# Optimization experiments

Hardware: AMD Instinct MI355X
Metric: run time of the kernel (lower is better)

## Reference

```python
import jax, jax.numpy as jnp
import numpy as np

N_HEAD = 16
N_EMBD = 1024
SPARSE_BLOCK = 64  # band width: keys j with i-64 <= j <= i are visible
B, T = 2, 2048


def setup_inputs() -> dict:
    key = jax.random.key(0)
    ks = jax.random.split(key, 5)
    C = N_EMBD
    scale = 0.02
    return {
        "x": jax.random.normal(ks[0], (B, T, C), dtype=jnp.float32),
        "Wqkv": jax.random.normal(ks[1], (C, 3 * C), dtype=jnp.float32) * scale,
        "bqkv": jnp.zeros((3 * C,), dtype=jnp.float32),
        "Wproj": jax.random.normal(ks[2], (C, C), dtype=jnp.float32) * scale,
        "bproj": jnp.zeros((C,), dtype=jnp.float32),
    }


def reference(x, Wqkv, bqkv, Wproj, bproj):
    Bz, Tz, C = x.shape
    H, D = N_HEAD, C // N_HEAD
    qkv = x @ Wqkv + bqkv                       # [B,T,3C]
    q, k, v = jnp.split(qkv, 3, axis=-1)

    def heads(t):  # [B,T,C] -> [B,H,T,D]
        return t.reshape(Bz, Tz, H, D).transpose(0, 2, 1, 3)
    q, k, v = heads(q), heads(k), heads(v)

    scale = 1.0 / jnp.sqrt(jnp.float32(D))
    att = jnp.einsum("bhtd,bhsd->bhts", q, k) * scale  # [B,H,T,T]

    # causal + local band mask: key j visible to query i iff i-64 <= j <= i
    i = jnp.arange(Tz)[:, None]
    j = jnp.arange(Tz)[None, :]
    mask = (j <= i) & (j >= i - SPARSE_BLOCK)           # [T,T] bool
    att = jnp.where(mask[None, None], att, -jnp.inf)
    att = jax.nn.softmax(att, axis=-1)

    y = jnp.einsum("bhts,bhsd->bhtd", att, v)           # [B,H,T,D]
    y = y.transpose(0, 2, 1, 3).reshape(Bz, Tz, C)
    return y @ Wproj + bproj
```

## Files before the change

kernel.cpp:

```cpp
#include <hip/hip_runtime.h>
#include <hip/hip_bf16.h>
#include <math.h>

#define N_HEAD 16
#define N_EMBD 1024
#define HEADD  64
#define BANDW  64
#define BB     2
#define TT     2048

typedef __attribute__((ext_vector_type(8))) short bf16x8;
typedef __attribute__((ext_vector_type(4))) float f32x4;

__device__ __forceinline__ ushort f2b(float f) {
    __hip_bfloat16 h = __float2bfloat16(f);
    union { __hip_bfloat16 h; ushort u; } cv; cv.h = h; return cv.u;
}
__device__ __forceinline__ float b2f(ushort u) { return __uint_as_float(((unsigned)u) << 16); }

#define GLOAD16(gp, lp) \
    __builtin_amdgcn_global_load_lds((const __attribute__((address_space(1))) void*)(gp), \
                                     (__attribute__((address_space(3))) void*)(lp), 16, 0, 0)

__global__ __launch_bounds__(256) void k_prep(
    const float* __restrict__ x, ushort* __restrict__ xb,
    const float* __restrict__ Wqkv, ushort* __restrict__ wqkvT,
    const float* __restrict__ Wproj, ushort* __restrict__ wprojT)
{
    __shared__ float tile[32][33];
    int bid = blockIdx.x;
    int t = threadIdx.x;
    if (bid < 4096) {
        int i = bid * 256 + t;
        float4 v = reinterpret_cast<const float4*>(x)[i];
        ushort4 o;
        o.x = f2b(v.x); o.y = f2b(v.y); o.z = f2b(v.z); o.w = f2b(v.w);
        reinterpret_cast<ushort4*>(xb)[i] = o;
        return;
    }
    const float* in; ushort* out; int R, C, bx, by;
    if (bid < 4096 + 3072) {
        int b2 = bid - 4096;
        in = Wqkv; out = wqkvT; R = 1024; C = 3072;
        bx = b2 % 96; by = b2 / 96;
    } else {
        int b3 = bid - 7168;
        in = Wproj; out = wprojT; R = 1024; C = 1024;
        bx = b3 & 31; by = b3 >> 5;
    }
    int tx = t & 31, ty = t >> 5;
    int c0 = bx * 32, r0 = by * 32;
    for (int rr = ty; rr < 32; rr += 8)
        tile[rr][tx] = in[(size_t)(r0 + rr) * C + (c0 + tx)];
    __syncthreads();
    for (int cc = ty; cc < 32; cc += 8)
        out[(size_t)(c0 + cc) * R + (r0 + tx)] = f2b(tile[tx][cc]);
}

template <bool OUT_BF16>
__global__ __launch_bounds__(512, 4) void k_gemm1(
    const ushort* __restrict__ A, const ushort* __restrict__ BT,
    const float* __restrict__ bias, void* __restrict__ Cout,
    int M, int N, int K)
{
    __shared__ __align__(16) char lds[81920];
    const int K2 = K * 2;
    int t = threadIdx.x, lane = t & 63, w = t >> 6;
    int wm = w >> 2, wn = w & 3;
    int lr = lane & 15, kg = lane >> 4;

    int nbx = N / 192;
    int cpx = gridDim.x >> 3;
    int wg = blockIdx.x;
    int wgid = (wg & 7) * cpx + (wg >> 3);
    int bx = wgid % nbx, by = wgid / nbx;
    int row0 = by * 128, col0 = bx * 192;

    size_t sA0, sA1, sB0, sB1, sB2;
    {
        int o = w * 2048 + lane * 16;
        int r = o >> 7, c = ((o >> 4) - r) & 7;
        sA0 = (size_t)r * K2 + c * 16;
        o += 1024; r = o >> 7; c = ((o >> 4) - r) & 7;
        sA1 = (size_t)r * K2 + c * 16;
        int ob = w * 3072 + lane * 16;
        int rb = ob >> 7, cb = ((ob >> 4) - rb) & 7;
        sB0 = (size_t)rb * K2 + cb * 16;
        ob += 1024; rb = ob >> 7; cb = ((ob >> 4) - rb) & 7;
        sB1 = (size_t)rb * K2 + cb * 16;
        ob += 1024; rb = ob >> 7; cb = ((ob >> 4) - rb) & 7;
        sB2 = (size_t)rb * K2 + cb * 16;
    }
    const char* gA = (const char*)A  + (size_t)row0 * K2;
    const char* gB = (const char*)BT + (size_t)col0 * K2;

    int offA[4][2], offB[3][2];
#pragma unroll
    for (int m = 0; m < 4; ++m) {
        int rr = wm * 64 + m * 16 + lr;
#pragma unroll
        for (int ks = 0; ks < 2; ++ks)
            offA[m][ks] = rr * 128 + (((ks * 4 + kg) + rr) & 7) * 16;
    }
#pragma unroll
    for (int n = 0; n < 3; ++n) {
        int rr = wn * 48 + n * 16 + lr;
#pragma unroll
        for (int ks = 0; ks < 2; ++ks)
            offB[n][ks] = rr * 128 + (((ks * 4 + kg) + rr) & 7) * 16;
    }

    f32x4 acc[4][3];
#pragma unroll
    for (int i = 0; i < 4; ++i)
#pragma unroll
        for (int j = 0; j < 3; ++j) { f32x4 z = {0.f, 0.f, 0.f, 0.f}; acc[i][j] = z; }

#define STAGE1(BUF, TI) do { \
        char* _db = lds + (BUF) * 40960; \
        const char* _ga = gA + (size_t)(TI) * 128; \
        const char* _gb = gB + (size_t)(TI) * 128; \
        GLOAD16(_ga + sA0, _db + w * 2048); \
        GLOAD16(_ga + sA1, _db + w * 2048 + 1024); \
        GLOAD16(_gb + sB0, _db + 16384 + w * 3072); \
        GLOAD16(_gb + sB1, _db + 16384 + w * 3072 + 1024); \
        GLOAD16(_gb + sB2, _db + 16384 + w * 3072 + 2048); \
    } while (0)

    int nt = K >> 6;
    STAGE1(0, 0);
    STAGE1(1, 1);
    asm volatile("s_waitcnt vmcnt(5)" ::: "memory");
    __builtin_amdgcn_s_barrier();

#pragma unroll 2
    for (int tt = 0; tt < nt; ++tt) {
        int cur = tt & 1;
        const char* bufb = lds + cur * 40960;
        bf16x8 af[4][2], bfr[3][2];
#pragma unroll
        for (int ks = 0; ks < 2; ++ks) {
#pragma unroll
            for (int m = 0; m < 4; ++m)
                af[m][ks] = *(const bf16x8*)(bufb + offA[m][ks]);
#pragma unroll
            for (int n = 0; n < 3; ++n)
                bfr[n][ks] = *(const bf16x8*)(bufb + 16384 + offB[n][ks]);
        }
        asm volatile("s_waitcnt lgkmcnt(0)" ::: "memory");
        __builtin_amdgcn_sched_barrier(0);
        __builtin_amdgcn_s_barrier();
        if (tt + 2 < nt) STAGE1(cur, tt + 2);
#pragma unroll
        for (int ks = 0; ks < 2; ++ks)
#pragma unroll
            for (int m = 0; m < 4; ++m)
#pragma unroll
                for (int n = 0; n < 3; ++n)
                    acc[m][n] = __builtin_amdgcn_mfma_f32_16x16x32_bf16(
                        af[m][ks], bfr[n][ks], acc[m][n], 0, 0, 0);
        if (tt + 2 < nt)
            asm volatile("s_waitcnt vmcnt(5)" ::: "memory");
        else
            asm volatile("s_waitcnt vmcnt(0)" ::: "memory");
        __builtin_amdgcn_s_barrier();
    }
#undef STAGE1

#pragma unroll
    for (int m = 0; m < 4; ++m) {
        int growb = row0 + wm * 64 + m * 16 + kg * 4;
#pragma unroll
        for (int n = 0; n < 3; ++n) {
            int gcol = col0 + wn * 48 + n * 16 + lr;
            float bv = bias ? bias[gcol] : 0.f;
#pragma unroll
            for (int e = 0; e < 4; ++e) {
                float val = acc[m][n][e] + bv;
                if (OUT_BF16)
                    ((ushort*)Cout)[(size_t)(growb + e) * N + gcol] = f2b(val);
                else
                    ((float*)Cout)[(size_t)(growb + e) * N + gcol] = val;
            }
        }
    }
}

template <bool OUT_BF16>
__global__ __launch_bounds__(256, 3) void k_gemm2(
    const ushort* __restrict__ A, const ushort* __restrict__ BT,
    const float* __restrict__ bias, void* __restrict__ Cout,
    int M, int N, int K)
{
    __shared__ __align__(16) char lds[2 * 24576];
    const int K2 = K * 2;
    int t = threadIdx.x, lane = t & 63, w = t >> 6;
    int wm = w >> 1, wn = w & 1;
    int lr = lane & 15, kg = lane >> 4;

    int nbx = N >> 6;
    int cpx = gridDim.x >> 3;
    int wg = blockIdx.x;
    int wgid = (wg & 7) * cpx + (wg >> 3);
    int bx = wgid % nbx, by = wgid / nbx;
    int row0 = by * 128, col0 = bx * 64;

    size_t sA[4], sB[2];
#pragma unroll
    for (int u = 0; u < 4; ++u) {
        int o = w * 4096 + u * 1024 + lane * 16;
        int r = o >> 7, c = ((o >> 4) - r) & 7;
        sA[u] = (size_t)r * K2 + c * 16;
    }
#pragma unroll
    for (int u = 0; u < 2; ++u) {
        int o = w * 2048 + u * 1024 + lane * 16;
        int r = o >> 7, c = ((o >> 4) - r) & 7;
        sB[u] = (size_t)r * K2 + c * 16;
    }
    const char* gA = (const char*)A  + (size_t)row0 * K2;
    const char* gB = (const char*)BT + (size_t)col0 * K2;

    int offA[4][2], offB[2][2];
#pragma unroll
    for (int m = 0; m < 4; ++m) {
        int rr = wm * 64 + m * 16 + lr;
#pragma unroll
        for (int ks = 0; ks < 2; ++ks)
            offA[m][ks] = rr * 128 + (((ks * 4 + kg) + rr) & 7) * 16;
    }
#pragma unroll
    for (int n = 0; n < 2; ++n) {
        int rr = wn * 32 + n * 16 + lr;
#pragma unroll
        for (int ks = 0; ks < 2; ++ks)
            offB[n][ks] = rr * 128 + (((ks * 4 + kg) + rr) & 7) * 16;
    }

    f32x4 acc[4][2];
#pragma unroll
    for (int i = 0; i < 4; ++i)
#pragma unroll
        for (int j = 0; j < 2; ++j) { f32x4 z = {0.f, 0.f, 0.f, 0.f}; acc[i][j] = z; }

#define STAGE2(BUF, TI) do { \
        char* _db = lds + (BUF) * 24576; \
        const char* _ga = gA + (size_t)(TI) * 128; \
        const char* _gb = gB + (size_t)(TI) * 128; \
        GLOAD16(_ga + sA[0], _db + w * 4096); \
        GLOAD16(_ga + sA[1], _db + w * 4096 + 1024); \
        GLOAD16(_ga + sA[2], _db + w * 4096 + 2048); \
        GLOAD16(_ga + sA[3], _db + w * 4096 + 3072); \
        GLOAD16(_gb + sB[0], _db + 16384 + w * 2048); \
        GLOAD16(_gb + sB[1], _db + 16384 + w * 2048 + 1024); \
    } while (0)

    int nt = K >> 6;
    STAGE2(0, 0);
    STAGE2(1, 1);
    asm volatile("s_waitcnt vmcnt(6)" ::: "memory");
    __builtin_amdgcn_s_barrier();

#pragma unroll 2
    for (int tt = 0; tt < nt; ++tt) {
        int cur = tt & 1;
        const char* bufb = lds + cur * 24576;
        bf16x8 af[4][2], bfr[2][2];
#pragma unroll
        for (int ks = 0; ks < 2; ++ks) {
#pragma unroll
            for (int m = 0; m < 4; ++m)
                af[m][ks] = *(const bf16x8*)(bufb + offA[m][ks]);
#pragma unroll
            for (int n = 0; n < 2; ++n)
                bfr[n][ks] = *(const bf16x8*)(bufb + 16384 + offB[n][ks]);
        }
        asm volatile("s_waitcnt lgkmcnt(0)" ::: "memory");
        __builtin_amdgcn_sched_barrier(0);
        __builtin_amdgcn_s_barrier();
        if (tt + 2 < nt) STAGE2(cur, tt + 2);
#pragma unroll
        for (int ks = 0; ks < 2; ++ks)
#pragma unroll
            for (int m = 0; m < 4; ++m)
#pragma unroll
                for (int n = 0; n < 2; ++n)
                    acc[m][n] = __builtin_amdgcn_mfma_f32_16x16x32_bf16(
                        af[m][ks], bfr[n][ks], acc[m][n], 0, 0, 0);
        if (tt + 2 < nt)
            asm volatile("s_waitcnt vmcnt(6)" ::: "memory");
        else
            asm volatile("s_waitcnt vmcnt(0)" ::: "memory");
        __builtin_amdgcn_s_barrier();
    }
#undef STAGE2

#pragma unroll
    for (int m = 0; m < 4; ++m) {
        int growb = row0 + wm * 64 + m * 16 + kg * 4;
#pragma unroll
        for (int n = 0; n < 2; ++n) {
            int gcol = col0 + wn * 32 + n * 16 + lr;
            float bv = bias ? bias[gcol] : 0.f;
#pragma unroll
            for (int e = 0; e < 4; ++e) {
                float val = acc[m][n][e] + bv;
                if (OUT_BF16)
                    ((ushort*)Cout)[(size_t)(growb + e) * N + gcol] = f2b(val);
                else
                    ((float*)Cout)[(size_t)(growb + e) * N + gcol] = val;
            }
        }
    }
}

__global__ __launch_bounds__(256) void k_attn(const ushort* __restrict__ qkv,
                                              ushort* __restrict__ y) {
    __shared__ __align__(16) ushort Ks[128 * 64];
    __shared__ ushort Vt[64][136];
    __shared__ ushort Ps[64][136];

    const int R3 = 3 * N_EMBD;
    int bid = blockIdx.x;
    int l  = (bid & 7) * 128 + (bid >> 3);
    int qt = l & 31;
    int h  = (l >> 5) & (N_HEAD - 1);
    int b  = l >> 9;
    int i0 = qt * 64;
    int j0 = i0 - BANDW;
    int hc = h * HEADD;

    int t    = threadIdx.x;
    int lane = t & 63;
    int wq   = t >> 6;
    int lr   = lane & 15;
    int kg   = lane >> 4;

    const ushort* kbase_g = qkv + (size_t)b * TT * R3 + N_EMBD + hc;
#pragma unroll
    for (int rnd = 0; rnd < 4; ++rnd) {
        int o = wq * 4096 + rnd * 1024 + lane * 16;
        int row  = o >> 7;
        int cblk = (((o >> 4) & 7) - row) & 7;
        int j = j0 + row; if (j < 0) j = 0;
        GLOAD16((const char*)(kbase_g + (size_t)j * R3) + cblk * 16,
                (char*)Ks + wq * 4096 + rnd * 1024);
    }

    {
        int row  = t >> 1;
        int part = t & 1;
        int j = j0 + row;
        if (j >= 0) {
            const ushort* vrow = qkv + (size_t)(b * TT + j) * R3 + 2 * N_EMBD + hc + part * 32;
#pragma unroll
            for (int c = 0; c < 4; ++c) {
                uint4 vv = reinterpret_cast<const uint4*>(vrow)[c];
                const ushort* pv = (const ushort*)&vv;
                int dbase = part * 32 + c * 8;
#pragma unroll
                for (int e = 0; e < 8; ++e)
                    Vt[dbase + e][row] = pv[e];
            }
        } else {
#pragma unroll
            for (int c = 0; c < 4; ++c) {
                int dbase = part * 32 + c * 8;
#pragma unroll
                for (int e = 0; e < 8; ++e)
                    Vt[dbase + e][row] = 0;
            }
        }
    }

    const ushort* qbase = qkv + (size_t)(b * TT + i0 + wq * 16 + lr) * R3 + hc;
    bf16x8 aq0 = *reinterpret_cast<const bf16x8*>(qbase + kg * 8);
    bf16x8 aq1 = *reinterpret_cast<const bf16x8*>(qbase + 32 + kg * 8);

    __syncthreads();

    f32x4 s[8];
#pragma unroll
    for (int nt = 0; nt < 8; ++nt) { f32x4 z = {0.f, 0.f, 0.f, 0.f}; s[nt] = z; }
#pragma unroll
    for (int nt = 0; nt < 8; ++nt) {
        int row = nt * 16 + lr;
        const char* kr = (const char*)Ks + row * 128;
        bf16x8 kb0 = *(const bf16x8*)(kr + (((kg)     + row) & 7) * 16);
        bf16x8 kb1 = *(const bf16x8*)(kr + (((4 + kg) + row) & 7) * 16);
        s[nt] = __builtin_amdgcn_mfma_f32_16x16x32_bf16(aq0, kb0, s[nt], 0, 0, 0);
        s[nt] = __builtin_amdgcn_mfma_f32_16x16x32_bf16(aq1, kb1, s[nt], 0, 0, 0);
    }

    float mx[4] = {-INFINITY, -INFINITY, -INFINITY, -INFINITY};
#pragma unroll
    for (int nt = 0; nt < 8; ++nt) {
        int kc = nt * 16 + lr;
#pragma unroll
        for (int e = 0; e < 4; ++e) {
            int qr = wq * 16 + kg * 4 + e;
            bool valid = (kc >= qr) && (kc <= qr + BANDW) && (j0 + kc >= 0);
            float v = s[nt][e] * 0.125f;
            s[nt][e] = valid ? v : -INFINITY;
            mx[e] = fmaxf(mx[e], s[nt][e]);
        }
    }
#pragma unroll
    for (int e = 0; e < 4; ++e) {
#pragma unroll
        for (int m = 1; m <= 8; m <<= 1)
            mx[e] = fmaxf(mx[e], __shfl_xor(mx[e], m, 64));
    }
    float sm[4] = {0.f, 0.f, 0.f, 0.f};
#pragma unroll
    for (int nt = 0; nt < 8; ++nt) {
        int kc = nt * 16 + lr;
#pragma unroll
        for (int e = 0; e < 4; ++e) {
            float p = __expf(s[nt][e] - mx[e]);
            sm[e] += p;
            Ps[wq * 16 + kg * 4 + e][kc] = f2b(p);
        }
    }
#pragma unroll
    for (int e = 0; e < 4; ++e) {
#pragma unroll
        for (int m = 1; m <= 8; m <<= 1)
            sm[e] += __shfl_xor(sm[e], m, 64);
    }

    f32x4 o[4];
#pragma unroll
    for (int vt = 0; vt < 4; ++vt) { f32x4 z = {0.f, 0.f, 0.f, 0.f}; o[vt] = z; }
#pragma unroll
    for (int ks = 0; ks < 4; ++ks) {
        bf16x8 pa = *reinterpret_cast<const bf16x8*>(&Ps[wq * 16 + lr][ks * 32 + kg * 8]);
#pragma unroll
        for (int vt = 0; vt < 4; ++vt) {
            bf16x8 vb = *reinterpret_cast<const bf16x8*>(&Vt[vt * 16 + lr][ks * 32 + kg * 8]);
            o[vt] = __builtin_amdgcn_mfma_f32_16x16x32_bf16(pa, vb, o[vt], 0, 0, 0);
        }
    }

    float inv[4];
#pragma unroll
    for (int e = 0; e < 4; ++e) inv[e] = 1.f / sm[e];

#pragma unroll
    for (int vt = 0; vt < 4; ++vt) {
#pragma unroll
        for (int e = 0; e < 4; ++e) {
            int qr = wq * 16 + kg * 4 + e;
            y[(size_t)(b * TT + i0 + qr) * N_EMBD + hc + vt * 16 + lr] =
                f2b(o[vt][e] * inv[e]);
        }
    }
}

extern "C" void kernel_launch(void* const* d_in, const int* in_sizes, int n_in,
                              void* d_out, int out_size, void* d_ws, size_t ws_size,
                              hipStream_t stream) {
    const float* x     = (const float*)d_in[0];
    const float* Wqkv  = (const float*)d_in[1];
    const float* bqkv  = (const float*)d_in[2];
    const float* Wproj = (const float*)d_in[3];
    const float* bproj = (const float*)d_in[4];
    float* out = (float*)d_out;

    const int M  = BB * TT;
    const int C  = N_EMBD;
    const int N1 = 3 * C;

    char* ws = (char*)d_ws;
    ushort* xb     = (ushort*)ws; ws += (size_t)M  * C * 2;
    ushort* wqkvT  = (ushort*)ws; ws += (size_t)N1 * C * 2;
    ushort* wprojT = (ushort*)ws; ws += (size_t)C  * C * 2;
    ushort* qkvb   = (ushort*)ws; ws += (size_t)M  * N1 * 2;
    ushort* yb     = (ushort*)ws; ws += (size_t)M  * C * 2;

    k_prep<<<8192, 256, 0, stream>>>(x, xb, Wqkv, wqkvT, Wproj, wprojT);
    {
        int nwg = (M / 128) * (N1 / 192);
        k_gemm1<true><<<nwg, 512, 0, stream>>>(xb, wqkvT, bqkv, (void*)qkvb, M, N1, C);
    }
    k_attn<<<BB * N_HEAD * (TT / 64), 256, 0, stream>>>(qkvb, yb);
    {
        int nwg = (M / 128) * (C / 64);
        k_gemm2<false><<<nwg, 256, 0, stream>>>(yb, wprojT, bproj, (void*)out, M, C, C);
    }
}
```

Before: 68.58 us.

## Fuse fp32-to-bf16 conversion of x into QKV GEMM A-tile loading

The separate pass that converts x to bf16 in k_prep is removed. The QKV GEMM now loads fp32 x directly into registers, converts it to bf16, and writes it to LDS while B still streams through global_load_lds. The output tile shrinks from 128x192 to 128x128 to make room in LDS and registers, which increases the workgroup count. This saves a full read and write of the bf16 copy of x, at the cost of reading twice as many bytes for A in the GEMM and doing conversion VALU work on the GEMM's critical path.

```diff
diff --git a/kernel.cpp b/kernel.cpp
--- a/kernel.cpp
+++ b/kernel.cpp
@@ -23,28 +23,18 @@
                                      (__attribute__((address_space(3))) void*)(lp), 16, 0, 0)
 
 __global__ __launch_bounds__(256) void k_prep(
-    const float* __restrict__ x, ushort* __restrict__ xb,
     const float* __restrict__ Wqkv, ushort* __restrict__ wqkvT,
     const float* __restrict__ Wproj, ushort* __restrict__ wprojT)
 {
     __shared__ float tile[32][33];
     int bid = blockIdx.x;
     int t = threadIdx.x;
-    if (bid < 4096) {
-        int i = bid * 256 + t;
-        float4 v = reinterpret_cast<const float4*>(x)[i];
-        ushort4 o;
-        o.x = f2b(v.x); o.y = f2b(v.y); o.z = f2b(v.z); o.w = f2b(v.w);
-        reinterpret_cast<ushort4*>(xb)[i] = o;
-        return;
-    }
     const float* in; ushort* out; int R, C, bx, by;
-    if (bid < 4096 + 3072) {
-        int b2 = bid - 4096;
+    if (bid < 3072) {
         in = Wqkv; out = wqkvT; R = 1024; C = 3072;
-        bx = b2 % 96; by = b2 / 96;
+        bx = bid % 96; by = bid / 96;
     } else {
-        int b3 = bid - 7168;
+        int b3 = bid - 3072;
         in = Wproj; out = wprojT; R = 1024; C = 1024;
         bx = b3 & 31; by = b3 >> 5;
     }
@@ -57,44 +47,53 @@
         out[(size_t)(c0 + cc) * R + (r0 + tx)] = f2b(tile[tx][cc]);
 }
 
+#define CVT8(CV, FA, FB) do { \
+    CV[0] = (short)f2b(FA[0]); CV[1] = (short)f2b(FA[1]); \
+    CV[2] = (short)f2b(FA[2]); CV[3] = (short)f2b(FA[3]); \
+    CV[4] = (short)f2b(FB[0]); CV[5] = (short)f2b(FB[1]); \
+    CV[6] = (short)f2b(FB[2]); CV[7] = (short)f2b(FB[3]); \
+} while (0)
+
 template <bool OUT_BF16>
 __global__ __launch_bounds__(512, 4) void k_gemm1(
-    const ushort* __restrict__ A, const ushort* __restrict__ BT,
+    const float* __restrict__ Xf, const ushort* __restrict__ BT,
     const float* __restrict__ bias, void* __restrict__ Cout,
     int M, int N, int K)
 {
-    __shared__ __align__(16) char lds[81920];
+    __shared__ __align__(16) char lds[2 * 32768];
     const int K2 = K * 2;
     int t = threadIdx.x, lane = t & 63, w = t >> 6;
     int wm = w >> 2, wn = w & 3;
     int lr = lane & 15, kg = lane >> 4;
 
-    int nbx = N / 192;
+    int nbx = N >> 7;
     int cpx = gridDim.x >> 3;
     int wg = blockIdx.x;
     int wgid = (wg & 7) * cpx + (wg >> 3);
     int bx = wgid % nbx, by = wgid / nbx;
-    int row0 = by * 128, col0 = bx * 192;
-
-    size_t sA0, sA1, sB0, sB1, sB2;
+    int row0 = by * 128, col0 = bx * 128;
+
+    unsigned voffA0, voffA1;
+    int oA0 = w * 2048 + lane * 16, oA1 = oA0 + 1024;
+    {
+        int r0 = oA0 >> 7, c0 = ((oA0 >> 4) - r0) & 7;
+        voffA0 = (unsigned)((row0 + r0) * (K * 4) + c0 * 32);
+        int r1 = oA1 >> 7, c1 = ((oA1 >> 4) - r1) & 7;
+        voffA1 = (unsigned)((row0 + r1) * (K * 4) + c1 * 32);
+    }
+    unsigned long xs = (unsigned long)Xf;
+
+    size_t sB0, sB1;
     {
         int o = w * 2048 + lane * 16;
         int r = o >> 7, c = ((o >> 4) - r) & 7;
-        sA0 = (size_t)r * K2 + c * 16;
+        sB0 = (size_t)r * K2 + c * 16;
         o += 1024; r = o >> 7; c = ((o >> 4) - r) & 7;
-        sA1 = (size_t)r * K2 + c * 16;
-        int ob = w * 3072 + lane * 16;
-        int rb = ob >> 7, cb = ((ob >> 4) - rb) & 7;
-        sB0 = (size_t)rb * K2 + cb * 16;
-        ob += 1024; rb = ob >> 7; cb = ((ob >> 4) - rb) & 7;
-        sB1 = (size_t)rb * K2 + cb * 16;
-        ob += 1024; rb = ob >> 7; cb = ((ob >> 4) - rb) & 7;
-        sB2 = (size_t)rb * K2 + cb * 16;
-    }
-    const char* gA = (const char*)A  + (size_t)row0 * K2;
+        sB1 = (size_t)r * K2 + c * 16;
+    }
     const char* gB = (const char*)BT + (size_t)col0 * K2;
 
-    int offA[4][2], offB[3][2];
+    int offA[4][2], offB[2][2];
 #pragma unroll
     for (int m = 0; m < 4; ++m) {
         int rr = wm * 64 + m * 16 + lr;
@@ -103,76 +102,108 @@
             offA[m][ks] = rr * 128 + (((ks * 4 + kg) + rr) & 7) * 16;
     }
 #pragma unroll
-    for (int n = 0; n < 3; ++n) {
-        int rr = wn * 48 + n * 16 + lr;
+    for (int n = 0; n < 2; ++n) {
+        int rr = wn * 32 + n * 16 + lr;
 #pragma unroll
         for (int ks = 0; ks < 2; ++ks)
-            offB[n][ks] = rr * 128 + (((ks * 4 + kg) + rr) & 7) * 16;
-    }
-
-    f32x4 acc[4][3];
+            offB[n][ks] = 16384 + rr * 128 + (((ks * 4 + kg) + rr) & 7) * 16;
+    }
+
+    f32x4 acc[4][2];
 #pragma unroll
     for (int i = 0; i < 4; ++i)
 #pragma unroll
-        for (int j = 0; j < 3; ++j) { f32x4 z = {0.f, 0.f, 0.f, 0.f}; acc[i][j] = z; }
-
-#define STAGE1(BUF, TI) do { \
-        char* _db = lds + (BUF) * 40960; \
-        const char* _ga = gA + (size_t)(TI) * 128; \
+        for (int j = 0; j < 2; ++j) { f32x4 z = {0.f, 0.f, 0.f, 0.f}; acc[i][j] = z; }
+
+#define LOADA(TI, F0, F1, F2, F3) do { \
+        unsigned _v0 = voffA0 + (unsigned)(TI) * 256u; \
+        unsigned _v1 = voffA1 + (unsigned)(TI) * 256u; \
+        asm volatile("global_load_dwordx4 %0, %1, %2"           : "=v"(F0) : "v"(_v0), "s"(xs) : "memory"); \
+        asm volatile("global_load_dwordx4 %0, %1, %2 offset:16" : "=v"(F1) : "v"(_v0), "s"(xs) : "memory"); \
+        asm volatile("global_load_dwordx4 %0, %1, %2"           : "=v"(F2) : "v"(_v1), "s"(xs) : "memory"); \
+        asm volatile("global_load_dwordx4 %0, %1, %2 offset:16" : "=v"(F3) : "v"(_v1), "s"(xs) : "memory"); \
+    } while (0)
+#define STGB(BUF, TI) do { \
+        char* _db = lds + (BUF) * 32768 + 16384; \
         const char* _gb = gB + (size_t)(TI) * 128; \
-        GLOAD16(_ga + sA0, _db + w * 2048); \
-        GLOAD16(_ga + sA1, _db + w * 2048 + 1024); \
-        GLOAD16(_gb + sB0, _db + 16384 + w * 3072); \
-        GLOAD16(_gb + sB1, _db + 16384 + w * 3072 + 1024); \
-        GLOAD16(_gb + sB2, _db + 16384 + w * 3072 + 2048); \
+        GLOAD16(_gb + sB0, _db + w * 2048); \
+        GLOAD16(_gb + sB1, _db + w * 2048 + 1024); \
     } while (0)
 
     int nt = K >> 6;
-    STAGE1(0, 0);
-    STAGE1(1, 1);
-    asm volatile("s_waitcnt vmcnt(5)" ::: "memory");
-    __builtin_amdgcn_s_barrier();
+    {
+        f32x4 p0, p1, p2, p3, p4, p5, p6, p7;
+        LOADA(0, p0, p1, p2, p3);
+        STGB(0, 0);
+        LOADA(1, p4, p5, p6, p7);
+        STGB(1, 1);
+        asm volatile("s_waitcnt vmcnt(2)" ::: "memory");
+        __builtin_amdgcn_sched_barrier(0);
+        bf16x8 c0, c1;
+        CVT8(c0, p0, p1); CVT8(c1, p2, p3);
+        *(bf16x8*)(lds + oA0) = c0;
+        *(bf16x8*)(lds + oA1) = c1;
+        CVT8(c0, p4, p5); CVT8(c1, p6, p7);
+        *(bf16x8*)(lds + 32768 + oA0) = c0;
+        *(bf16x8*)(lds + 32768 + oA1) = c1;
+        asm volatile("s_waitcnt lgkmcnt(0)" ::: "memory");
+        __builtin_amdgcn_s_barrier();
+    }
 
 #pragma unroll 2
     for (int tt = 0; tt < nt; ++tt) {
         int cur = tt & 1;
-        const char* bufb = lds + cur * 40960;
-        bf16x8 af[4][2], bfr[3][2];
+        char* bufb = lds + cur * 32768;
+        bf16x8 af[4][2], bfr[2][2];
 #pragma unroll
         for (int ks = 0; ks < 2; ++ks) {
 #pragma unroll
             for (int m = 0; m < 4; ++m)
                 af[m][ks] = *(const bf16x8*)(bufb + offA[m][ks]);
 #pragma unroll
-            for (int n = 0; n < 3; ++n)
-                bfr[n][ks] = *(const bf16x8*)(bufb + 16384 + offB[n][ks]);
+            for (int n = 0; n < 2; ++n)
+                bfr[n][ks] = *(const bf16x8*)(bufb + offB[n][ks]);
         }
         asm volatile("s_waitcnt lgkmcnt(0)" ::: "memory");
         __builtin_amdgcn_sched_barrier(0);
         __builtin_amdgcn_s_barrier();
-        if (tt + 2 < nt) STAGE1(cur, tt + 2);
+        bool st = (tt + 2 < nt);
+        f32x4 q0, q1, q2, q3;
+        if (st) {
+            LOADA(tt + 2, q0, q1, q2, q3);
+            STGB(cur, tt + 2);
+        }
 #pragma unroll
         for (int ks = 0; ks < 2; ++ks)
 #pragma unroll
             for (int m = 0; m < 4; ++m)
 #pragma unroll
-                for (int n = 0; n < 3; ++n)
+                for (int n = 0; n < 2; ++n)
                     acc[m][n] = __builtin_amdgcn_mfma_f32_16x16x32_bf16(
                         af[m][ks], bfr[n][ks], acc[m][n], 0, 0, 0);
-        if (tt + 2 < nt)
-            asm volatile("s_waitcnt vmcnt(5)" ::: "memory");
+        if (st)
+            asm volatile("s_waitcnt vmcnt(2)" ::: "memory");
         else
             asm volatile("s_waitcnt vmcnt(0)" ::: "memory");
+        __builtin_amdgcn_sched_barrier(0);
+        if (st) {
+            bf16x8 c0, c1;
+            CVT8(c0, q0, q1); CVT8(c1, q2, q3);
+            *(bf16x8*)(bufb + oA0) = c0;
+            *(bf16x8*)(bufb + oA1) = c1;
+        }
+        asm volatile("s_waitcnt lgkmcnt(0)" ::: "memory");
         __builtin_amdgcn_s_barrier();
     }
-#undef STAGE1
+#undef LOADA
+#undef STGB
 
 #pragma unroll
     for (int m = 0; m < 4; ++m) {
         int growb = row0 + wm * 64 + m * 16 + kg * 4;
 #pragma unroll
-        for (int n = 0; n < 3; ++n) {
-            int gcol = col0 + wn * 48 + n * 16 + lr;
+        for (int n = 0; n < 2; ++n) {
+            int gcol = col0 + wn * 32 + n * 16 + lr;
             float bv = bias ? bias[gcol] : 0.f;
 #pragma unroll
             for (int e = 0; e < 4; ++e) {
@@ -472,16 +503,15 @@
     const int N1 = 3 * C;
 
     char* ws = (char*)d_ws;
-    ushort* xb     = (ushort*)ws; ws += (size_t)M  * C * 2;
     ushort* wqkvT  = (ushort*)ws; ws += (size_t)N1 * C * 2;
     ushort* wprojT = (ushort*)ws; ws += (size_t)C  * C * 2;
     ushort* qkvb   = (ushort*)ws; ws += (size_t)M  * N1 * 2;
     ushort* yb     = (ushort*)ws; ws += (size_t)M  * C * 2;
 
-    k_prep<<<8192, 256, 0, stream>>>(x, xb, Wqkv, wqkvT, Wproj, wprojT);
+    k_prep<<<4096, 256, 0, stream>>>(Wqkv, wqkvT, Wproj, wprojT);
     {
-        int nwg = (M / 128) * (N1 / 192);
-        k_gemm1<true><<<nwg, 512, 0, stream>>>(xb, wqkvT, bqkv, (void*)qkvb, M, N1, C);
+        int nwg = (M / 128) * (N1 / 128);
+        k_gemm1<true><<<nwg, 512, 0, stream>>>(x, wqkvT, bqkv, (void*)qkvb, M, N1, C);
     }
     k_attn<<<BB * N_HEAD * (TT / 64), 256, 0, stream>>>(qkvb, yb);
     {
```

Result: slower. 82.69 us (+20.6%).
